# Performance work log

Hardware: AMD Instinct MI355X
Metric: run time of the kernel (lower is better)

## Reference

```python
import jax, jax.numpy as jnp
import numpy as np

N_HEADS = 16
ROPE_DIMS = 64


def _rope_tables(T, rd):
    # freqs: 1 / 10000^(arange(0, rd, 2)/rd), shape [rd//2]
    freqs = 1.0 / (10000.0 ** (np.arange(0, rd, 2, dtype=np.float32) / np.float32(rd)))
    ang = np.outer(np.arange(T, dtype=np.float32), freqs)  # [T, rd//2]
    return jnp.asarray(np.cos(ang)), jnp.asarray(np.sin(ang))


def _apply_rope(x, cos, sin, rd):
    # x: [B, H, T, D]; rotate-half style on first rd dims
    x_rope, x_pass = x[..., :rd], x[..., rd:]
    x1, x2 = x_rope[..., : rd // 2], x_rope[..., rd // 2 :]
    c = cos[None, None]  # [1,1,T,rd//2]
    s = sin[None, None]
    x_rot = jnp.concatenate([x1 * c - x2 * s, x2 * c + x1 * s], axis=-1)
    return jnp.concatenate([x_rot, x_pass], axis=-1)


def setup_inputs() -> dict:
    key = jax.random.key(0)
    k1, k2, k3 = jax.random.split(key, 3)
    B, T, C = 32, 512, 2048
    x = jax.random.normal(k1, (B, T, C), dtype=jnp.float32)
    w_qkv = jax.random.normal(k2, (3 * C, C), dtype=jnp.float32) * 0.02
    w_out = jax.random.normal(k3, (C, C), dtype=jnp.float32) * 0.02
    return {"x": x, "w_qkv": w_qkv, "w_out": w_out}


def reference(x, w_qkv, w_out):
    B, T, C = x.shape
    H = N_HEADS
    D = C // H
    # fused QKV projection: F.linear(x, w) = x @ w.T
    qkv = jnp.einsum('btc,fc->btf', x, w_qkv).reshape(B, T, 3, H, D)
    q = jnp.transpose(qkv[:, :, 0], (0, 2, 1, 3))  # [B,H,T,D]
    k = jnp.transpose(qkv[:, :, 1], (0, 2, 1, 3))
    v = jnp.transpose(qkv[:, :, 2], (0, 2, 1, 3))
    cos, sin = _rope_tables(T, ROPE_DIMS)
    q = _apply_rope(q, cos, sin, ROPE_DIMS)
    k = _apply_rope(k, cos, sin, ROPE_DIMS)
    # causal SDPA
    scale = 1.0 / jnp.sqrt(jnp.asarray(D, dtype=x.dtype))
    scores = jnp.einsum('bhqd,bhkd->bhqk', q, k) * scale
    causal = jnp.tril(jnp.ones((T, T), dtype=bool))
    scores = jnp.where(causal[None, None], scores, jnp.finfo(scores.dtype).min)
    attn = jax.nn.softmax(scores, axis=-1)
    y = jnp.einsum('bhqk,bhkd->bhqd', attn, v)
    y = jnp.transpose(y, (0, 2, 1, 3)).reshape(B, T, C)
    return jnp.einsum('btc,fc->btf', y, w_out)
```

## Files before the change

kernel.cpp:

```cpp
#include <hip/hip_runtime.h>


typedef __bf16 bf16x8 __attribute__((ext_vector_type(8)));
typedef float floatx4 __attribute__((ext_vector_type(4)));

__device__ __forceinline__ unsigned short f2bf(float f) {
  union { float f; unsigned u; } v; v.f = f;
  unsigned r = v.u + 0x7FFFu + ((v.u >> 16) & 1u);
  return (unsigned short)(r >> 16);
}
__device__ __forceinline__ float bf2f(unsigned short h) {
  union { unsigned u; float f; } v; v.u = ((unsigned)h) << 16; return v.f;
}

__device__ __forceinline__ void load_lds16(const void* g, void* l) {
  __builtin_amdgcn_global_load_lds((__attribute__((address_space(1))) void*)g,
                                   (__attribute__((address_space(3))) void*)l,
                                   16, 0, 0);
}

__global__ void rope_tables(float* __restrict__ cost, float* __restrict__ sint) {
  int i = blockIdx.x * 256 + threadIdx.x;
  if (i >= 512 * 32) return;
  int t = i >> 5, f = i & 31;
  float e = -(float)(2 * f) / 64.0f;
  float freq = powf(10000.0f, e);
  float ang = (float)t * freq;
  cost[i] = cosf(ang);
  sint[i] = sinf(ang);
}

__global__ void cast_bf16(const float* __restrict__ in,
                          unsigned short* __restrict__ out, int n8) {
  int i = blockIdx.x * 256 + threadIdx.x;
  if (i >= n8) return;
  float4 a = ((const float4*)in)[2 * i];
  float4 b = ((const float4*)in)[2 * i + 1];
  union { uint4 v; unsigned short u[8]; } o;
  o.u[0] = f2bf(a.x); o.u[1] = f2bf(a.y); o.u[2] = f2bf(a.z); o.u[3] = f2bf(a.w);
  o.u[4] = f2bf(b.x); o.u[5] = f2bf(b.y); o.u[6] = f2bf(b.z); o.u[7] = f2bf(b.w);
  ((uint4*)out)[i] = o.v;
}

template <int OUT_BF16>
__global__ __launch_bounds__(256) void gemm_bt(
    const unsigned short* __restrict__ A, const unsigned short* __restrict__ Bt,
    void* __restrict__ Cout, int M, int N, int K) {
  __shared__ __align__(16) unsigned short As[128 * 64];
  __shared__ __align__(16) unsigned short Bs[128 * 64];
  const int tid = threadIdx.x;
  const int bn = blockIdx.x, bm = blockIdx.y;
  const int w = tid >> 6, l = tid & 63;
  const int quad = l >> 4, cl = l & 15;
  const int m_base = (w & 1) * 64, n_base = (w >> 1) * 64;
  floatx4 acc[4][4] = {};

  const int srow = tid >> 3;
  const int sc = (tid & 7) ^ (srow & 7);
  const unsigned short* Ag = A + (size_t)(bm * 128 + srow) * K + sc * 8;
  const unsigned short* Bg = Bt + (size_t)(bn * 128 + srow) * K + sc * 8;
  unsigned short* asd = As + tid * 8;
  unsigned short* bsd = Bs + tid * 8;

  for (int kt = 0; kt < K; kt += 64) {
    __syncthreads();
#pragma unroll
    for (int i = 0; i < 4; ++i) {
      load_lds16(Ag + (size_t)i * 32 * K + kt, asd + i * 32 * 64);
      load_lds16(Bg + (size_t)i * 32 * K + kt, bsd + i * 32 * 64);
    }
    __syncthreads();
#pragma unroll
    for (int k0 = 0; k0 < 64; k0 += 32) {
      const int xs = (((k0 >> 3) + quad) ^ (cl & 7)) << 3;
      bf16x8 a[4], b[4];
#pragma unroll
      for (int mt = 0; mt < 4; ++mt)
        a[mt] = *(const bf16x8*)(As + (m_base + mt * 16 + cl) * 64 + xs);
#pragma unroll
      for (int nt = 0; nt < 4; ++nt)
        b[nt] = *(const bf16x8*)(Bs + (n_base + nt * 16 + cl) * 64 + xs);
#pragma unroll
      for (int mt = 0; mt < 4; ++mt)
#pragma unroll
        for (int nt = 0; nt < 4; ++nt)
          acc[mt][nt] = __builtin_amdgcn_mfma_f32_16x16x32_bf16(
              a[mt], b[nt], acc[mt][nt], 0, 0, 0);
    }
  }
#pragma unroll
  for (int mt = 0; mt < 4; ++mt)
#pragma unroll
    for (int nt = 0; nt < 4; ++nt)
#pragma unroll
      for (int r = 0; r < 4; ++r) {
        int gm = bm * 128 + m_base + mt * 16 + quad * 4 + r;
        int gn = bn * 128 + n_base + nt * 16 + cl;
        float v = acc[mt][nt][r];
        if (OUT_BF16)
          ((unsigned short*)Cout)[(size_t)gm * N + gn] = f2bf(v);
        else
          ((float*)Cout)[(size_t)gm * N + gn] = v;
      }
}

__global__ __launch_bounds__(256) void attn_kernel(
    const unsigned short* __restrict__ qkv, const float* __restrict__ cost,
    const float* __restrict__ sint, unsigned short* __restrict__ y) {
  __shared__ __align__(16) unsigned short Qs[64][136];
  __shared__ __align__(16) unsigned short Ks[64][136];
  __shared__ __align__(16) unsigned short VTs[128][64];
  __shared__ __align__(16) unsigned short Ps[4][16][72];

  const int bh = blockIdx.x, qt = blockIdx.y;
  const int b = bh >> 4, h = bh & 15;
  const int tid = threadIdx.x, w = tid >> 6, l = tid & 63;
  const int quad = l >> 4, cl = l & 15;
  const float scale = 0.08838834764831845f * 1.4426950408889634f;

  {
    const int r = tid >> 2, j = tid & 3;
    const int tg = qt * 64 + r;
    const unsigned short* qrow = qkv + (size_t)(b * 512 + tg) * 6144 + h * 128;
    union { uint4 v; unsigned short u[8]; } c1, c2, p1, p2, o1, o2, o3, o4;
    c1.v = *(const uint4*)(qrow + j * 8);
    c2.v = *(const uint4*)(qrow + j * 8 + 32);
    p1.v = *(const uint4*)(qrow + 64 + j * 16);
    p2.v = *(const uint4*)(qrow + 64 + j * 16 + 8);
#pragma unroll
    for (int jj = 0; jj < 8; ++jj) {
      int d = j * 8 + jj;
      float c = cost[tg * 32 + d], s = sint[tg * 32 + d];
      float x1 = bf2f(c1.u[jj]), x2 = bf2f(c2.u[jj]);
      o1.u[jj] = f2bf((x1 * c - x2 * s) * scale);
      o2.u[jj] = f2bf((x2 * c + x1 * s) * scale);
      o3.u[jj] = f2bf(bf2f(p1.u[jj]) * scale);
      o4.u[jj] = f2bf(bf2f(p2.u[jj]) * scale);
    }
    *(uint4*)&Qs[r][j * 8]          = o1.v;
    *(uint4*)&Qs[r][j * 8 + 32]     = o2.v;
    *(uint4*)&Qs[r][64 + j * 16]     = o3.v;
    *(uint4*)&Qs[r][64 + j * 16 + 8] = o4.v;
  }

  floatx4 o[8] = {};
  float m_i[4] = {-__builtin_inff(), -__builtin_inff(), -__builtin_inff(),
                  -__builtin_inff()};
  float l_i[4] = {0.f, 0.f, 0.f, 0.f};

  for (int ktile = 0; ktile <= qt; ++ktile) {
    __syncthreads();
    {
      const int r = tid >> 2, j = tid & 3;
      const int tg = ktile * 64 + r;
      const unsigned short* krow =
          qkv + (size_t)(b * 512 + tg) * 6144 + 2048 + h * 128;
      union { uint4 v; unsigned short u[8]; } c1, c2, p1, p2, o1, o2;
      c1.v = *(const uint4*)(krow + j * 8);
      c2.v = *(const uint4*)(krow + j * 8 + 32);
      p1.v = *(const uint4*)(krow + 64 + j * 16);
      p2.v = *(const uint4*)(krow + 64 + j * 16 + 8);
#pragma unroll
      for (int jj = 0; jj < 8; ++jj) {
        int d = j * 8 + jj;
        float c = cost[tg * 32 + d], s = sint[tg * 32 + d];
        float x1 = bf2f(c1.u[jj]), x2 = bf2f(c2.u[jj]);
        o1.u[jj] = f2bf(x1 * c - x2 * s);
        o2.u[jj] = f2bf(x2 * c + x1 * s);
      }
      *(uint4*)&Ks[r][j * 8]          = o1.v;
      *(uint4*)&Ks[r][j * 8 + 32]     = o2.v;
      *(uint4*)&Ks[r][64 + j * 16]     = p1.v;
      *(uint4*)&Ks[r][64 + j * 16 + 8] = p2.v;
    }
    {
      const int rowg = tid >> 5;
      const int colg = tid & 31;
      const int kk0 = rowg * 8, d0 = colg * 4;
      const unsigned short* vbase = qkv +
          (size_t)(b * 512 + ktile * 64 + kk0) * 6144 + 4096 + h * 128 + d0;
      uint2 rv[8];
#pragma unroll
      for (int rr = 0; rr < 8; ++rr)
        rv[rr] = *(const uint2*)(vbase + (size_t)rr * 6144);
#pragma unroll
      for (int c = 0; c < 4; ++c) {
        const int d = d0 + c;
        unsigned out[4];
#pragma unroll
        for (int p = 0; p < 4; ++p) {
          unsigned ua = ((const unsigned*)&rv[2 * p])[c >> 1];
          unsigned ub = ((const unsigned*)&rv[2 * p + 1])[c >> 1];
          unsigned lo = (c & 1) ? (ua >> 16) : (ua & 0xffffu);
          unsigned hi = (c & 1) ? (ub >> 16) : (ub & 0xffffu);
          out[p] = lo | (hi << 16);
        }
        *(uint4*)&VTs[d][(rowg ^ (d & 7)) << 3] = *(uint4*)out;
      }
    }
    __syncthreads();

    floatx4 s[4] = {};
#pragma unroll
    for (int kc = 0; kc < 4; ++kc) {
      bf16x8 aq = *(const bf16x8*)(&Qs[w * 16 + cl][kc * 32 + quad * 8]);
#pragma unroll
      for (int nt = 0; nt < 4; ++nt) {
        bf16x8 bk = *(const bf16x8*)(&Ks[nt * 16 + cl][kc * 32 + quad * 8]);
        s[nt] = __builtin_amdgcn_mfma_f32_16x16x32_bf16(aq, bk, s[nt], 0, 0, 0);
      }
    }
    if (ktile == qt) {
#pragma unroll
      for (int nt = 0; nt < 4; ++nt)
#pragma unroll
        for (int r = 0; r < 4; ++r) {
          int qrow_l = w * 16 + quad * 4 + r;
          int kcol_l = nt * 16 + cl;
          if (kcol_l > qrow_l) s[nt][r] = -__builtin_inff();
        }
    }
#pragma unroll
    for (int r = 0; r < 4; ++r) {
      float mx = fmaxf(fmaxf(s[0][r], s[1][r]), fmaxf(s[2][r], s[3][r]));
      mx = fmaxf(mx, __shfl_xor(mx, 1));
      mx = fmaxf(mx, __shfl_xor(mx, 2));
      mx = fmaxf(mx, __shfl_xor(mx, 4));
      mx = fmaxf(mx, __shfl_xor(mx, 8));
      float mn = fmaxf(m_i[r], mx);
      float a = exp2f(m_i[r] - mn);
      float rs = 0.f;
#pragma unroll
      for (int nt = 0; nt < 4; ++nt) {
        float p = exp2f(s[nt][r] - mn);
        s[nt][r] = p;
        rs += p;
      }
      rs += __shfl_xor(rs, 1);
      rs += __shfl_xor(rs, 2);
      rs += __shfl_xor(rs, 4);
      rs += __shfl_xor(rs, 8);
      l_i[r] = l_i[r] * a + rs;
      m_i[r] = mn;
#pragma unroll
      for (int nt2 = 0; nt2 < 8; ++nt2) o[nt2][r] *= a;
#pragma unroll
      for (int nt = 0; nt < 4; ++nt)
        Ps[w][quad * 4 + r][nt * 16 + cl] = f2bf(s[nt][r]);
    }
    __syncthreads();

#pragma unroll
    for (int kc2 = 0; kc2 < 2; ++kc2) {
      bf16x8 ap = *(const bf16x8*)(&Ps[w][cl][kc2 * 32 + quad * 8]);
#pragma unroll
      for (int nt2 = 0; nt2 < 8; ++nt2) {
        bf16x8 bv = *(const bf16x8*)(
            &VTs[nt2 * 16 + cl][((kc2 * 4 + quad) ^ (cl & 7)) << 3]);
        o[nt2] = __builtin_amdgcn_mfma_f32_16x16x32_bf16(ap, bv, o[nt2], 0, 0, 0);
      }
    }
  }

#pragma unroll
  for (int r = 0; r < 4; ++r) {
    float inv = 1.0f / l_i[r];
    size_t row =
        (size_t)(b * 512 + qt * 64 + w * 16 + quad * 4 + r) * 2048 + h * 128;
#pragma unroll
    for (int nt2 = 0; nt2 < 8; ++nt2)
      y[row + nt2 * 16 + cl] = f2bf(o[nt2][r] * inv);
  }
}

extern "C" void kernel_launch(void* const* d_in, const int* in_sizes, int n_in,
                              void* d_out, int out_size, void* d_ws,
                              size_t ws_size, hipStream_t stream) {
  const float* x = (const float*)d_in[0];
  const float* wqkv = (const float*)d_in[1];
  const float* wout = (const float*)d_in[2];
  float* out = (float*)d_out;

  char* ws = (char*)d_ws;
  float* cost = (float*)ws;            ws += (size_t)512 * 32 * 4;
  float* sint = (float*)ws;            ws += (size_t)512 * 32 * 4;
  unsigned short* xb = (unsigned short*)ws;    ws += (size_t)16384 * 2048 * 2;
  unsigned short* wqkvb = (unsigned short*)ws; ws += (size_t)6144 * 2048 * 2;
  unsigned short* woutb = (unsigned short*)ws; ws += (size_t)2048 * 2048 * 2;
  unsigned short* qkvb = (unsigned short*)ws;  ws += (size_t)16384 * 6144 * 2;
  unsigned short* yb = (unsigned short*)ws;    ws += (size_t)16384 * 2048 * 2;

  rope_tables<<<dim3(64), dim3(256), 0, stream>>>(cost, sint);
  cast_bf16<<<dim3(16384), dim3(256), 0, stream>>>(x, xb, 33554432 / 8);
  cast_bf16<<<dim3(6144), dim3(256), 0, stream>>>(wqkv, wqkvb, 12582912 / 8);
  cast_bf16<<<dim3(2048), dim3(256), 0, stream>>>(wout, woutb, 4194304 / 8);
  gemm_bt<1><<<dim3(48, 128), dim3(256), 0, stream>>>(xb, wqkvb, (void*)qkvb,
                                                      16384, 6144, 2048);
  attn_kernel<<<dim3(512, 8), dim3(256), 0, stream>>>(qkvb, cost, sint, yb);
  gemm_bt<0><<<dim3(16, 128), dim3(256), 0, stream>>>(yb, woutb, (void*)out,
                                                      16384, 2048, 2048);
}
```

Before: 1.056 ms.

## Precompute RoPE and V transpose in separate passes, stream K/V via direct LDS loads

RoPE and Q scaling now run once in a separate in-place pass over the QKV buffer, and V is pre-transposed into a separate buffer that reuses the x bf16 scratch. The attention kernel no longer repeats RoPE and the V transpose for every query tile. It keeps Q fragments in registers and fills swizzled K/V tiles with global_load_lds direct copies. The cost is two extra kernel launches and an extra read and write pass over Q, K and V in global memory.

```diff
diff --git a/kernel.cpp b/kernel.cpp
--- a/kernel.cpp
+++ b/kernel.cpp
@@ -40,6 +40,79 @@
   o.u[0] = f2bf(a.x); o.u[1] = f2bf(a.y); o.u[2] = f2bf(a.z); o.u[3] = f2bf(a.w);
   o.u[4] = f2bf(b.x); o.u[5] = f2bf(b.y); o.u[6] = f2bf(b.z); o.u[7] = f2bf(b.w);
   ((uint4*)out)[i] = o.v;
+}
+
+__global__ __launch_bounds__(256) void rope_qk(
+    unsigned short* __restrict__ qkv, const float* __restrict__ cost,
+    const float* __restrict__ sint) {
+  const int bid = blockIdx.x;
+  const int is_k = bid >= 8192;
+  const int gr = (bid & 8191) * 32 + (threadIdx.x >> 3);
+  const int j = threadIdx.x & 7;
+  const int bt = gr >> 4, h = gr & 15, t = bt & 511;
+  unsigned short* p =
+      qkv + (size_t)bt * 6144 + h * 128 + (is_k ? 2048 : 0);
+  const float qscale = 0.08838834764831845f * 1.4426950408889634f;
+  if (j < 4) {
+    union { uint4 v; unsigned short u[8]; } a, bb, oa, ob;
+    a.v = *(const uint4*)(p + j * 8);
+    bb.v = *(const uint4*)(p + j * 8 + 32);
+    float4 c0 = *(const float4*)(cost + t * 32 + j * 8);
+    float4 c1 = *(const float4*)(cost + t * 32 + j * 8 + 4);
+    float4 s0 = *(const float4*)(sint + t * 32 + j * 8);
+    float4 s1 = *(const float4*)(sint + t * 32 + j * 8 + 4);
+    float cs[8] = {c0.x, c0.y, c0.z, c0.w, c1.x, c1.y, c1.z, c1.w};
+    float sn[8] = {s0.x, s0.y, s0.z, s0.w, s1.x, s1.y, s1.z, s1.w};
+    const float sc = is_k ? 1.0f : qscale;
+#pragma unroll
+    for (int jj = 0; jj < 8; ++jj) {
+      float x1 = bf2f(a.u[jj]), x2 = bf2f(bb.u[jj]);
+      oa.u[jj] = f2bf((x1 * cs[jj] - x2 * sn[jj]) * sc);
+      ob.u[jj] = f2bf((x2 * cs[jj] + x1 * sn[jj]) * sc);
+    }
+    *(uint4*)(p + j * 8) = oa.v;
+    *(uint4*)(p + j * 8 + 32) = ob.v;
+  } else if (!is_k) {
+#pragma unroll
+    for (int cc = 0; cc < 2; ++cc) {
+      const int chunk = j + 4 + cc * 4;
+      union { uint4 v; unsigned short u[8]; } a, oa;
+      a.v = *(const uint4*)(p + chunk * 8);
+#pragma unroll
+      for (int jj = 0; jj < 8; ++jj) oa.u[jj] = f2bf(bf2f(a.u[jj]) * qscale);
+      *(uint4*)(p + chunk * 8) = oa.v;
+    }
+  }
+}
+
+__global__ __launch_bounds__(256) void transpose_v(
+    const unsigned short* __restrict__ qkv, unsigned short* __restrict__ vT) {
+  const int bh = blockIdx.x, tt = blockIdx.y;
+  const int b = bh >> 4, h = bh & 15;
+  const int rowg = threadIdx.x & 7;
+  const int colg = threadIdx.x >> 3;
+  const int d0 = colg * 4;
+  const unsigned short* vbase = qkv +
+      (size_t)(b * 512 + tt * 64 + rowg * 8) * 6144 + 4096 + h * 128 + d0;
+  uint2 rv[8];
+#pragma unroll
+  for (int rr = 0; rr < 8; ++rr)
+    rv[rr] = *(const uint2*)(vbase + (size_t)rr * 6144);
+#pragma unroll
+  for (int c = 0; c < 4; ++c) {
+    const int d = d0 + c;
+    unsigned out[4];
+#pragma unroll
+    for (int p = 0; p < 4; ++p) {
+      unsigned ua = ((const unsigned*)&rv[2 * p])[c >> 1];
+      unsigned ub = ((const unsigned*)&rv[2 * p + 1])[c >> 1];
+      unsigned lo = (c & 1) ? (ua >> 16) : (ua & 0xffffu);
+      unsigned hi = (c & 1) ? (ub >> 16) : (ub & 0xffffu);
+      out[p] = lo | (hi << 16);
+    }
+    *(uint4*)(vT + ((size_t)bh * 128 + d) * 512 + tt * 64 + rowg * 8) =
+        *(uint4*)out;
+  }
 }
 
 template <int OUT_BF16>
@@ -105,43 +178,33 @@
 }
 
 __global__ __launch_bounds__(256) void attn_kernel(
-    const unsigned short* __restrict__ qkv, const float* __restrict__ cost,
-    const float* __restrict__ sint, unsigned short* __restrict__ y) {
-  __shared__ __align__(16) unsigned short Qs[64][136];
-  __shared__ __align__(16) unsigned short Ks[64][136];
-  __shared__ __align__(16) unsigned short VTs[128][64];
+    const unsigned short* __restrict__ qkv, const unsigned short* __restrict__ vT,
+    unsigned short* __restrict__ y) {
+  __shared__ __align__(16) unsigned short Ks[64 * 128];
+  __shared__ __align__(16) unsigned short VTs[128 * 64];
   __shared__ __align__(16) unsigned short Ps[4][16][72];
 
   const int bh = blockIdx.x, qt = blockIdx.y;
   const int b = bh >> 4, h = bh & 15;
   const int tid = threadIdx.x, w = tid >> 6, l = tid & 63;
   const int quad = l >> 4, cl = l & 15;
-  const float scale = 0.08838834764831845f * 1.4426950408889634f;
-
-  {
-    const int r = tid >> 2, j = tid & 3;
-    const int tg = qt * 64 + r;
-    const unsigned short* qrow = qkv + (size_t)(b * 512 + tg) * 6144 + h * 128;
-    union { uint4 v; unsigned short u[8]; } c1, c2, p1, p2, o1, o2, o3, o4;
-    c1.v = *(const uint4*)(qrow + j * 8);
-    c2.v = *(const uint4*)(qrow + j * 8 + 32);
-    p1.v = *(const uint4*)(qrow + 64 + j * 16);
-    p2.v = *(const uint4*)(qrow + 64 + j * 16 + 8);
-#pragma unroll
-    for (int jj = 0; jj < 8; ++jj) {
-      int d = j * 8 + jj;
-      float c = cost[tg * 32 + d], s = sint[tg * 32 + d];
-      float x1 = bf2f(c1.u[jj]), x2 = bf2f(c2.u[jj]);
-      o1.u[jj] = f2bf((x1 * c - x2 * s) * scale);
-      o2.u[jj] = f2bf((x2 * c + x1 * s) * scale);
-      o3.u[jj] = f2bf(bf2f(p1.u[jj]) * scale);
-      o4.u[jj] = f2bf(bf2f(p2.u[jj]) * scale);
-    }
-    *(uint4*)&Qs[r][j * 8]          = o1.v;
-    *(uint4*)&Qs[r][j * 8 + 32]     = o2.v;
-    *(uint4*)&Qs[r][64 + j * 16]     = o3.v;
-    *(uint4*)&Qs[r][64 + j * 16 + 8] = o4.v;
-  }
+
+  const unsigned short* qrow =
+      qkv + (size_t)(b * 512 + qt * 64 + w * 16 + cl) * 6144 + h * 128;
+  bf16x8 aq[4];
+#pragma unroll
+  for (int kc = 0; kc < 4; ++kc)
+    aq[kc] = *(const bf16x8*)(qrow + kc * 32 + quad * 8);
+
+  const int srK = tid >> 4;
+  const int scK = (tid & 15) ^ (srK & 7);
+  const unsigned short* Kg =
+      qkv + (size_t)(b * 512 + srK) * 6144 + 2048 + h * 128 + scK * 8;
+  unsigned short* Kd = Ks + tid * 8;
+  const int srV = tid >> 3;
+  const int scV = (tid & 7) ^ (srV & 7);
+  const unsigned short* Vg = vT + ((size_t)bh * 128 + srV) * 512 + scV * 8;
+  unsigned short* Vd = VTs + tid * 8;
 
   floatx4 o[8] = {};
   float m_i[4] = {-__builtin_inff(), -__builtin_inff(), -__builtin_inff(),
@@ -150,66 +213,23 @@
 
   for (int ktile = 0; ktile <= qt; ++ktile) {
     __syncthreads();
-    {
-      const int r = tid >> 2, j = tid & 3;
-      const int tg = ktile * 64 + r;
-      const unsigned short* krow =
-          qkv + (size_t)(b * 512 + tg) * 6144 + 2048 + h * 128;
-      union { uint4 v; unsigned short u[8]; } c1, c2, p1, p2, o1, o2;
-      c1.v = *(const uint4*)(krow + j * 8);
-      c2.v = *(const uint4*)(krow + j * 8 + 32);
-      p1.v = *(const uint4*)(krow + 64 + j * 16);
-      p2.v = *(const uint4*)(krow + 64 + j * 16 + 8);
-#pragma unroll
-      for (int jj = 0; jj < 8; ++jj) {
-        int d = j * 8 + jj;
-        float c = cost[tg * 32 + d], s = sint[tg * 32 + d];
-        float x1 = bf2f(c1.u[jj]), x2 = bf2f(c2.u[jj]);
-        o1.u[jj] = f2bf(x1 * c - x2 * s);
-        o2.u[jj] = f2bf(x2 * c + x1 * s);
+#pragma unroll
+    for (int i = 0; i < 4; ++i) {
+      load_lds16(Kg + (size_t)(ktile * 64 + i * 16) * 6144, Kd + i * 2048);
+      load_lds16(Vg + (size_t)i * 32 * 512 + ktile * 64, Vd + i * 2048);
+    }
+    __syncthreads();
+
+    floatx4 s[4] = {};
+#pragma unroll
+    for (int kc = 0; kc < 4; ++kc)
+#pragma unroll
+      for (int nt = 0; nt < 4; ++nt) {
+        bf16x8 bk = *(const bf16x8*)(
+            Ks + (nt * 16 + cl) * 128 + (((kc * 4 + quad) ^ (cl & 7)) << 3));
+        s[nt] = __builtin_amdgcn_mfma_f32_16x16x32_bf16(aq[kc], bk, s[nt],
+                                                        0, 0, 0);
       }
-      *(uint4*)&Ks[r][j * 8]          = o1.v;
-      *(uint4*)&Ks[r][j * 8 + 32]     = o2.v;
-      *(uint4*)&Ks[r][64 + j * 16]     = p1.v;
-      *(uint4*)&Ks[r][64 + j * 16 + 8] = p2.v;
-    }
-    {
-      const int rowg = tid >> 5;
-      const int colg = tid & 31;
-      const int kk0 = rowg * 8, d0 = colg * 4;
-      const unsigned short* vbase = qkv +
-          (size_t)(b * 512 + ktile * 64 + kk0) * 6144 + 4096 + h * 128 + d0;
-      uint2 rv[8];
-#pragma unroll
-      for (int rr = 0; rr < 8; ++rr)
-        rv[rr] = *(const uint2*)(vbase + (size_t)rr * 6144);
-#pragma unroll
-      for (int c = 0; c < 4; ++c) {
-        const int d = d0 + c;
-        unsigned out[4];
-#pragma unroll
-        for (int p = 0; p < 4; ++p) {
-          unsigned ua = ((const unsigned*)&rv[2 * p])[c >> 1];
-          unsigned ub = ((const unsigned*)&rv[2 * p + 1])[c >> 1];
-          unsigned lo = (c & 1) ? (ua >> 16) : (ua & 0xffffu);
-          unsigned hi = (c & 1) ? (ub >> 16) : (ub & 0xffffu);
-          out[p] = lo | (hi << 16);
-        }
-        *(uint4*)&VTs[d][(rowg ^ (d & 7)) << 3] = *(uint4*)out;
-      }
-    }
-    __syncthreads();
-
-    floatx4 s[4] = {};
-#pragma unroll
-    for (int kc = 0; kc < 4; ++kc) {
-      bf16x8 aq = *(const bf16x8*)(&Qs[w * 16 + cl][kc * 32 + quad * 8]);
-#pragma unroll
-      for (int nt = 0; nt < 4; ++nt) {
-        bf16x8 bk = *(const bf16x8*)(&Ks[nt * 16 + cl][kc * 32 + quad * 8]);
-        s[nt] = __builtin_amdgcn_mfma_f32_16x16x32_bf16(aq, bk, s[nt], 0, 0, 0);
-      }
-    }
     if (ktile == qt) {
 #pragma unroll
       for (int nt = 0; nt < 4; ++nt)
@@ -256,8 +276,9 @@
 #pragma unroll
       for (int nt2 = 0; nt2 < 8; ++nt2) {
         bf16x8 bv = *(const bf16x8*)(
-            &VTs[nt2 * 16 + cl][((kc2 * 4 + quad) ^ (cl & 7)) << 3]);
-        o[nt2] = __builtin_amdgcn_mfma_f32_16x16x32_bf16(ap, bv, o[nt2], 0, 0, 0);
+            VTs + (nt2 * 16 + cl) * 64 + (((kc2 * 4 + quad) ^ (cl & 7)) << 3));
+        o[nt2] = __builtin_amdgcn_mfma_f32_16x16x32_bf16(ap, bv, o[nt2],
+                                                         0, 0, 0);
       }
     }
   }
@@ -289,6 +310,7 @@
   unsigned short* woutb = (unsigned short*)ws; ws += (size_t)2048 * 2048 * 2;
   unsigned short* qkvb = (unsigned short*)ws;  ws += (size_t)16384 * 6144 * 2;
   unsigned short* yb = (unsigned short*)ws;    ws += (size_t)16384 * 2048 * 2;
+  unsigned short* vT = xb;
 
   rope_tables<<<dim3(64), dim3(256), 0, stream>>>(cost, sint);
   cast_bf16<<<dim3(16384), dim3(256), 0, stream>>>(x, xb, 33554432 / 8);
@@ -296,7 +318,9 @@
   cast_bf16<<<dim3(2048), dim3(256), 0, stream>>>(wout, woutb, 4194304 / 8);
   gemm_bt<1><<<dim3(48, 128), dim3(256), 0, stream>>>(xb, wqkvb, (void*)qkvb,
                                                       16384, 6144, 2048);
-  attn_kernel<<<dim3(512, 8), dim3(256), 0, stream>>>(qkvb, cost, sint, yb);
+  rope_qk<<<dim3(16384), dim3(256), 0, stream>>>(qkvb, cost, sint);
+  transpose_v<<<dim3(512, 8), dim3(256), 0, stream>>>(qkvb, vT);
+  attn_kernel<<<dim3(512, 8), dim3(256), 0, stream>>>(qkvb, vT, yb);
   gemm_bt<0><<<dim3(16, 128), dim3(256), 0, stream>>>(yb, woutb, (void*)out,
                                                       16384, 2048, 2048);
 }
```

Result: no change. 1.064 ms (+0.8%).
